# Kernel optimization log

Measured on AMD Instinct MI355X. Metric: run time of the kernel, lower is better.

The kernel has to match this reference:

```python
import jax, jax.numpy as jnp
import numpy as np

N_NODES = 100000
N_EDGES = 1600000
D = 128  # feat_input_size_node == embed_inside_size == feat_target_size


def gcn_layer(x, W, b, row, col, ew, n_nodes):
    """PyG GCNConv with scalar edge_weight, add_self_loops=True, normalize=True.
    x: [N, Fin], W: [Fout, Fin], b: [Fout], row/col: [E], ew: [E].
    Messages flow row -> col (source_to_target)."""
    h = x @ W.T  # [N, Fout]
    # degree includes self-loop weight 1.0 per node
    deg = jax.ops.segment_sum(ew, col, num_segments=n_nodes) + 1.0  # [N]
    dinv = jnp.where(deg > 0, jax.lax.rsqrt(deg), 0.0)  # [N]
    norm = dinv[row] * ew * dinv[col]  # [E]
    msgs = norm[:, None] * h[row]  # [E, Fout] -- gather
    agg = jax.ops.segment_sum(msgs, col, num_segments=n_nodes)  # scatter-add
    agg = agg + (dinv * dinv)[:, None] * h  # self-loop contribution (weight 1)
    return agg + b


def setup_inputs() -> dict:
    key = jax.random.key(0)
    k1, k2, k3, k4, k5, k6, k7 = jax.random.split(key, 7)
    edge_tuples = jax.random.randint(k1, (2, N_EDGES), 0, N_NODES, dtype=jnp.int64) if jax.config.jax_enable_x64 else jax.random.randint(k1, (2, N_EDGES), 0, N_NODES).astype(jnp.int32)
    edge_feats = jax.random.uniform(k2, (N_EDGES, 1), dtype=jnp.float32)
    node_feats = jax.random.normal(k3, (N_NODES, D), dtype=jnp.float32)
    s1 = 1.0 / np.sqrt(D)
    W1 = jax.random.uniform(k4, (D, D), minval=-s1, maxval=s1, dtype=jnp.float32)
    b1 = jnp.zeros((D,), dtype=jnp.float32)
    W2 = jax.random.uniform(k5, (D, D), minval=-s1, maxval=s1, dtype=jnp.float32)
    b2 = jnp.zeros((D,), dtype=jnp.float32)
    return {"edge_tuples": edge_tuples, "edge_feats": edge_feats, "node_feats": node_feats,
            "W1": W1, "b1": b1, "W2": W2, "b2": b2}


def reference(edge_tuples, edge_feats, node_feats, W1, b1, W2, b2):
    row, col = edge_tuples[0], edge_tuples[1]
    ew = edge_feats.squeeze(-1)  # [E]
    n = node_feats.shape[0]
    h = gcn_layer(node_feats, W1, b1, row, col, ew, n)
    h = jnp.tanh(h)  # activate='tanh' between the two GCN layers
    out = gcn_layer(h, W2, b2, row, col, ew, n)
    # skip=Identity (Fin==Fout), doskip=1
    return out + node_feats
```

## Files before the change

kernel.cpp:

```cpp
#include <hip/hip_runtime.h>
#include <hip/hip_bf16.h>
#include <math.h>

#define D 128
#define SCAN_T 256
#define EPB 4096
#define MAXNB 800

typedef unsigned long long ull;
typedef unsigned short ushort_t;
typedef __attribute__((ext_vector_type(8))) short bf16x8;
typedef __attribute__((ext_vector_type(4))) float f32x4;

__device__ __forceinline__ float bf_lo(unsigned u) { return __uint_as_float(u << 16); }
__device__ __forceinline__ float bf_hi(unsigned u) { return __uint_as_float(u & 0xffff0000u); }
__device__ __forceinline__ unsigned bpack(float a, float b) {
  unsigned ua = __float_as_uint(a), ub = __float_as_uint(b);
  ua += 0x7fff + ((ua >> 16) & 1);
  ub += 0x7fff + ((ub >> 16) & 1);
  return (ua >> 16) | (ub & 0xffff0000u);
}
__device__ __forceinline__ ushort_t bh16(float a) {
  unsigned ua = __float_as_uint(a);
  ua += 0x7fff + ((ua >> 16) & 1);
  return (ushort_t)(ua >> 16);
}

__global__ __launch_bounds__(256) void k_h1(const int* __restrict__ col, int E, int B1, int B1pad,
                                            int* __restrict__ gh, int NB,
                                            const float2* __restrict__ x2, unsigned* __restrict__ xb, int n64,
                                            const float* __restrict__ W1, const float* __restrict__ W2,
                                            ushort_t* __restrict__ Whi1, ushort_t* __restrict__ Wlo1,
                                            ushort_t* __restrict__ Whi2, ushort_t* __restrict__ Wlo2) {
  int b = blockIdx.x, t = threadIdx.x;
  if (b < B1) {
    __shared__ int h[MAXNB];
    for (int i = t; i < NB; i += 256) h[i] = 0;
    __syncthreads();
    int e0 = b * EPB, e1 = min(E, e0 + EPB);
    for (int e = e0 + t; e < e1; e += 256) atomicAdd(&h[col[e] >> 7], 1);
    __syncthreads();
    for (int i = t; i < NB; i += 256) gh[i * B1pad + b] = h[i];
    return;
  }
  int idx = (b - B1) * 256 + t;
  if (idx < n64) { float2 v = x2[idx]; xb[idx] = bpack(v.x, v.y); return; }
  int j = idx - n64;
  if (j >= 2 * D * D) return;
  const float* W = (j < D * D) ? W1 : W2;
  ushort_t* Hh = (j < D * D) ? Whi1 : Whi2;
  ushort_t* Hl = (j < D * D) ? Wlo1 : Wlo2;
  int k = j & (D * D - 1);
  float w = W[k];
  ushort_t hh = bh16(w);
  Hh[k] = hh;
  Hl[k] = bh16(w - __uint_as_float((unsigned)hh << 16));
}

__global__ __launch_bounds__(512) void k_hscan(int* __restrict__ gh, int* __restrict__ binTotal,
                                               int B1, int B1pad) {
  __shared__ int wsum[8];
  int bin = blockIdx.x, t = threadIdx.x;
  int v = (t < B1) ? gh[bin * B1pad + t] : 0;
  int lane = t & 63, wid = t >> 6;
  int x = v;
  #pragma unroll
  for (int d = 1; d < 64; d <<= 1) { int y = __shfl_up(x, d, 64); if (lane >= d) x += y; }
  if (lane == 63) wsum[wid] = x;
  __syncthreads();
  int woff = 0;
  for (int w = 0; w < wid; ++w) woff += wsum[w];
  if (t < B1) gh[bin * B1pad + t] = woff + x - v;
  if (t == 511) binTotal[bin] = woff + x;
}

__device__ __forceinline__ int block_excl_scan(int v, int t, int* wsum, int* total) {
  int lane = t & 63, wid = t >> 6;
  int x = v;
  #pragma unroll
  for (int d = 1; d < 64; d <<= 1) {
    int y = __shfl_up(x, d, 64);
    if (lane >= d) x += y;
  }
  if (lane == 63) wsum[wid] = x;
  __syncthreads();
  int woff = 0;
  for (int w = 0; w < wid; ++w) woff += wsum[w];
  if (total) { int tot = 0; for (int w = 0; w < 4; ++w) tot += wsum[w]; *total = tot; }
  return woff + x - v;
}

__global__ __launch_bounds__(SCAN_T) void k_hscan2(const int* __restrict__ binTotal,
                                                   int* __restrict__ binBase, int NB) {
  __shared__ int wsum[4];
  int t = threadIdx.x;
  int base = t * 4;
  int v[4]; int s = 0;
  #pragma unroll
  for (int u = 0; u < 4; ++u) { v[u] = (base + u < NB) ? binTotal[base + u] : 0; s += v[u]; }
  int tot;
  int excl = block_excl_scan(s, t, wsum, &tot);
  int run = excl;
  #pragma unroll
  for (int u = 0; u < 4; ++u) { if (base + u < NB) binBase[base + u] = run; run += v[u]; }
  if (t == 0) binBase[NB] = tot;
}

__global__ __launch_bounds__(256) void k_scatter(const int* __restrict__ row, const int* __restrict__ col,
                                                 const float* __restrict__ ew,
                                                 const int* __restrict__ gh, const int* __restrict__ binBase,
                                                 int B1pad, int NB,
                                                 ull* __restrict__ a_e, int E) {
  __shared__ ull recs[EPB];
  __shared__ int hist[MAXNB];
  __shared__ int cur[MAXNB];
  __shared__ int wb[MAXNB];
  __shared__ int wsum[4];
  int b = blockIdx.x, t = threadIdx.x;
  for (int i = t; i < NB; i += 256) { hist[i] = 0; cur[i] = 0; }
  __syncthreads();
  int e0 = b * EPB;
  int cnt = min(E - e0, EPB);
  ull v[16];
  #pragma unroll
  for (int k = 0; k < 16; ++k) {
    int idx = t + k * 256;
    v[k] = 0;
    if (idx < cnt) {
      int e = e0 + idx;
      int c = col[e];
      unsigned q = __float2uint_rn(ew[e] * 32767.0f);
      if (q > 32767u) q = 32767u;
      unsigned hi = ((unsigned)c << 15) | q;
      v[k] = ((ull)hi << 32) | (unsigned)row[e];
      atomicAdd(&hist[hi >> 22], 1);
    }
  }
  __syncthreads();
  int base = t * 4;
  int hv[4];
  #pragma unroll
  for (int u = 0; u < 4; ++u) hv[u] = (base + u < NB) ? hist[base + u] : 0;
  int s = hv[0] + hv[1] + hv[2] + hv[3];
  int excl = block_excl_scan(s, t, wsum, nullptr);
  int run = excl;
  #pragma unroll
  for (int u = 0; u < 4; ++u) {
    if (base + u < NB) {
      hist[base + u] = run;
      wb[base + u] = binBase[base + u] + gh[(base + u) * B1pad + b] - run;
    }
    run += hv[u];
  }
  __syncthreads();
  #pragma unroll
  for (int k = 0; k < 16; ++k) {
    if (t + k * 256 < cnt) {
      unsigned bkt = (unsigned)(v[k] >> 54);
      int idx = hist[bkt] + atomicAdd(&cur[bkt], 1);
      recs[idx] = v[k];
    }
  }
  __syncthreads();
  for (int i = t; i < cnt; i += 256) {
    ull r = recs[i];
    a_e[wb[(unsigned)(r >> 54)] + i] = r;
  }
}

__global__ __launch_bounds__(256) void k_bucket(const ull* __restrict__ a_e,
                                                const int* __restrict__ binBase,
                                                int* __restrict__ offs, float* __restrict__ deg,
                                                unsigned* __restrict__ sorted2, int N) {
  __shared__ int hist[128];
  __shared__ float wdeg[128];
  __shared__ int pfx[128];
  __shared__ int cur[128];
  int bin = blockIdx.x, t = threadIdx.x;
  if (t < 128) { hist[t] = 0; wdeg[t] = 0.f; cur[t] = 0; }
  __syncthreads();
  int s0 = binBase[bin], s1 = binBase[bin + 1];
  for (int i = s0 + t; i < s1; i += 256) {
    unsigned hi = (unsigned)(a_e[i] >> 32);
    int lc = (hi >> 15) & 127;
    atomicAdd(&hist[lc], 1);
    atomicAdd(&wdeg[lc], (float)(hi & 32767u) * (1.0f / 32767.0f));
  }
  __syncthreads();
  if (t == 0) { int run = 0; for (int i = 0; i < 128; ++i) { pfx[i] = run; run += hist[i]; } }
  __syncthreads();
  int c0 = bin << 7;
  if (t < 128 && c0 + t < N) { offs[c0 + t] = s0 + pfx[t]; deg[c0 + t] = wdeg[t]; }
  for (int i = s0 + t; i < s1; i += 256) {
    ull v = a_e[i];
    unsigned hi = (unsigned)(v >> 32);
    int lc = (hi >> 15) & 127;
    int pos = s0 + pfx[lc] + atomicAdd(&cur[lc], 1);
    sorted2[pos] = ((unsigned)v << 15) | (hi & 32767u);
  }
}

__global__ void k_dinv(const float* __restrict__ deg, float* __restrict__ dinv,
                       int* __restrict__ offs, int N, int E) {
  int i = blockIdx.x * blockDim.x + threadIdx.x;
  if (i == 0) offs[N] = E;
  if (i < N) dinv[i] = rsqrtf(deg[i] + 1.0f);
}

__global__ void k_norm(unsigned* __restrict__ el, const int* __restrict__ offs,
                       const float* __restrict__ dinv, int N) {
  int c = blockIdx.x * blockDim.x + threadIdx.x;
  if (c >= N) return;
  int s0 = offs[c], s1 = offs[c + 1];
  float dc = dinv[c] * (1.0f / 32767.0f);
  for (int i = s0; i < s1; ++i) {
    unsigned v = el[i];
    unsigned r = v >> 15;
    float nrm = dinv[r] * (float)(v & 32767u) * dc;
    unsigned q = __float2uint_rn(nrm * 32767.0f);
    if (q > 32767u) q = 32767u;
    el[i] = (r << 15) | q;
  }
}

__global__ __launch_bounds__(256) void k_agg(const unsigned* __restrict__ H2,
                                             const unsigned* __restrict__ elist,
                                             const int* __restrict__ offs, const float* __restrict__ dinv,
                                             unsigned* __restrict__ outb, int N) {
  int lane = threadIdx.x & 63;
  int c = blockIdx.x * 4 + (threadIdx.x >> 6);
  if (c >= N) return;
  int start = offs[c];
  int m = offs[c + 1] - start;
  int q = lane >> 4;
  int fi = lane & 15;
  float a0 = 0.f, a1 = 0.f, a2 = 0.f, a3 = 0.f, a4 = 0.f, a5 = 0.f, a6 = 0.f, a7 = 0.f;
  for (int base = 0; base < m; base += 64) {
    int chunk = min(64, m - base);
    unsigned rec = (lane < chunk) ? elist[start + base + lane] : 0u;
    int iters = (chunk + 3) >> 2;
    int i = 0;
    for (; i + 4 <= iters; i += 4) {
      unsigned e0 = __shfl(rec, 4 * i + q, 64);
      unsigned e1 = __shfl(rec, 4 * i + 4 + q, 64);
      unsigned e2 = __shfl(rec, 4 * i + 8 + q, 64);
      unsigned e3 = __shfl(rec, 4 * i + 12 + q, 64);
      uint4 u0 = *(const uint4*)&H2[(size_t)(e0 >> 15) * 64 + fi * 4];
      uint4 u1 = *(const uint4*)&H2[(size_t)(e1 >> 15) * 64 + fi * 4];
      uint4 u2 = *(const uint4*)&H2[(size_t)(e2 >> 15) * 64 + fi * 4];
      uint4 u3 = *(const uint4*)&H2[(size_t)(e3 >> 15) * 64 + fi * 4];
      float w0 = (float)(e0 & 0x7fffu) * (1.0f / 32767.0f);
      float w1 = (float)(e1 & 0x7fffu) * (1.0f / 32767.0f);
      float w2 = (float)(e2 & 0x7fffu) * (1.0f / 32767.0f);
      float w3 = (float)(e3 & 0x7fffu) * (1.0f / 32767.0f);
      a0 += w0 * bf_lo(u0.x); a1 += w0 * bf_hi(u0.x);
      a2 += w0 * bf_lo(u0.y); a3 += w0 * bf_hi(u0.y);
      a4 += w0 * bf_lo(u0.z); a5 += w0 * bf_hi(u0.z);
      a6 += w0 * bf_lo(u0.w); a7 += w0 * bf_hi(u0.w);
      a0 += w1 * bf_lo(u1.x); a1 += w1 * bf_hi(u1.x);
      a2 += w1 * bf_lo(u1.y); a3 += w1 * bf_hi(u1.y);
      a4 += w1 * bf_lo(u1.z); a5 += w1 * bf_hi(u1.z);
      a6 += w1 * bf_lo(u1.w); a7 += w1 * bf_hi(u1.w);
      a0 += w2 * bf_lo(u2.x); a1 += w2 * bf_hi(u2.x);
      a2 += w2 * bf_lo(u2.y); a3 += w2 * bf_hi(u2.y);
      a4 += w2 * bf_lo(u2.z); a5 += w2 * bf_hi(u2.z);
      a6 += w2 * bf_lo(u2.w); a7 += w2 * bf_hi(u2.w);
      a0 += w3 * bf_lo(u3.x); a1 += w3 * bf_hi(u3.x);
      a2 += w3 * bf_lo(u3.y); a3 += w3 * bf_hi(u3.y);
      a4 += w3 * bf_lo(u3.z); a5 += w3 * bf_hi(u3.z);
      a6 += w3 * bf_lo(u3.w); a7 += w3 * bf_hi(u3.w);
    }
    for (; i < iters; ++i) {
      unsigned e0 = __shfl(rec, 4 * i + q, 64);
      float w0 = (float)(e0 & 0x7fffu) * (1.0f / 32767.0f);
      uint4 u0 = *(const uint4*)&H2[(size_t)(e0 >> 15) * 64 + fi * 4];
      a0 += w0 * bf_lo(u0.x); a1 += w0 * bf_hi(u0.x);
      a2 += w0 * bf_lo(u0.y); a3 += w0 * bf_hi(u0.y);
      a4 += w0 * bf_lo(u0.z); a5 += w0 * bf_hi(u0.z);
      a6 += w0 * bf_lo(u0.w); a7 += w0 * bf_hi(u0.w);
    }
  }
  a0 += __shfl_xor(a0, 16, 64); a0 += __shfl_xor(a0, 32, 64);
  a1 += __shfl_xor(a1, 16, 64); a1 += __shfl_xor(a1, 32, 64);
  a2 += __shfl_xor(a2, 16, 64); a2 += __shfl_xor(a2, 32, 64);
  a3 += __shfl_xor(a3, 16, 64); a3 += __shfl_xor(a3, 32, 64);
  a4 += __shfl_xor(a4, 16, 64); a4 += __shfl_xor(a4, 32, 64);
  a5 += __shfl_xor(a5, 16, 64); a5 += __shfl_xor(a5, 32, 64);
  a6 += __shfl_xor(a6, 16, 64); a6 += __shfl_xor(a6, 32, 64);
  a7 += __shfl_xor(a7, 16, 64); a7 += __shfl_xor(a7, 32, 64);
  if (q == 0) {
    float dv = dinv[c], sw = dv * dv;
    uint4 us = *(const uint4*)&H2[(size_t)c * 64 + fi * 4];
    a0 += sw * bf_lo(us.x); a1 += sw * bf_hi(us.x);
    a2 += sw * bf_lo(us.y); a3 += sw * bf_hi(us.y);
    a4 += sw * bf_lo(us.z); a5 += sw * bf_hi(us.z);
    a6 += sw * bf_lo(us.w); a7 += sw * bf_hi(us.w);
    uint4 o;
    o.x = bpack(a0, a1); o.y = bpack(a2, a3); o.z = bpack(a4, a5); o.w = bpack(a6, a7);
    *(uint4*)&outb[(size_t)c * 64 + fi * 4] = o;
  }
}

template<int TANH, int SKIP>
__global__ __launch_bounds__(256) void k_mgemm(const ushort_t* __restrict__ S,
                                               const ushort_t* __restrict__ Whi,
                                               const ushort_t* __restrict__ Wlo,
                                               const float* __restrict__ bias,
                                               const ushort_t* __restrict__ skipb,
                                               void* __restrict__ outv, int n) {
  int wave = threadIdx.x >> 6, lane = threadIdx.x & 63;
  int cl = lane & 15;
  int kg = lane >> 4;
  int cb0 = wave * 2;

  bf16x8 bh[2][4], bl[2][4];
  float bv[2];
  #pragma unroll
  for (int c = 0; c < 2; ++c) {
    int col = (cb0 + c) * 16 + cl;
    const ushort_t* wh = Whi + (size_t)col * D + kg * 8;
    const ushort_t* wl = Wlo + (size_t)col * D + kg * 8;
    #pragma unroll
    for (int kt = 0; kt < 4; ++kt) {
      bh[c][kt] = *(const bf16x8*)(wh + kt * 32);
      bl[c][kt] = *(const bf16x8*)(wl + kt * 32);
    }
    bv[c] = bias[col];
  }

  int ntiles = (n + 15) >> 4;
  for (int t = blockIdx.x; t < ntiles; t += gridDim.x) {
    int arow = t * 16 + cl; if (arow >= n) arow = n - 1;
    const ushort_t* srow = S + (size_t)arow * D + kg * 8;
    bf16x8 a[4];
    #pragma unroll
    for (int kt = 0; kt < 4; ++kt) a[kt] = *(const bf16x8*)(srow + kt * 32);
    #pragma unroll
    for (int c = 0; c < 2; ++c) {
      f32x4 acc = {0.f, 0.f, 0.f, 0.f};
      #pragma unroll
      for (int kt = 0; kt < 4; ++kt)
        acc = __builtin_amdgcn_mfma_f32_16x16x32_bf16(a[kt], bh[c][kt], acc, 0, 0, 0);
      #pragma unroll
      for (int kt = 0; kt < 4; ++kt)
        acc = __builtin_amdgcn_mfma_f32_16x16x32_bf16(a[kt], bl[c][kt], acc, 0, 0, 0);
      int col = (cb0 + c) * 16 + cl;
      #pragma unroll
      for (int i = 0; i < 4; ++i) {
        int r = t * 16 + kg * 4 + i;
        if (r < n) {
          float o = acc[i] + bv[c];
          if (TANH) {
            o = tanhf(o);
            ((ushort_t*)outv)[(size_t)r * D + col] = bh16(o);
          } else {
            if (SKIP) o += __uint_as_float((unsigned)skipb[(size_t)r * D + col] << 16);
            ((float*)outv)[(size_t)r * D + col] = o;
          }
        }
      }
    }
  }
}

extern "C" void kernel_launch(void* const* d_in, const int* in_sizes, int n_in,
                              void* d_out, int out_size, void* d_ws, size_t ws_size,
                              hipStream_t stream) {
  const int*   et = (const int*)d_in[0];
  const float* ef = (const float*)d_in[1];
  const float* x  = (const float*)d_in[2];
  const float* W1 = (const float*)d_in[3];
  const float* b1 = (const float*)d_in[4];
  const float* W2 = (const float*)d_in[5];
  const float* b2 = (const float*)d_in[6];

  int E = in_sizes[1];
  int N = in_sizes[2] / D;
  const int* row = et;
  const int* col = et + E;

  int NB = (N + 127) >> 7;
  int B1 = (E + EPB - 1) / EPB;
  int B1pad = (B1 + 7) & ~7;

  char* p = (char*)d_ws;
  auto alloc = [&](size_t bytes) { char* q = p; p += (bytes + 255) & ~(size_t)255; return q; };
  int*      gh       = (int*)     alloc((size_t)NB * B1pad * 4);
  int*      binTotal = (int*)     alloc((size_t)NB * 4);
  int*      binBase  = (int*)     alloc((size_t)(NB + 1) * 4);
  ull*      a_e      = (ull*)     alloc((size_t)E * 8);
  unsigned* elist    = (unsigned*)alloc((size_t)E * 4);
  int*      offs     = (int*)     alloc((size_t)(N + 1) * 4);
  float*    deg      = (float*)   alloc((size_t)N * 4);
  float*    dinv     = (float*)   alloc((size_t)N * 4);
  unsigned* xb       = (unsigned*)alloc((size_t)N * 64 * 4);
  unsigned* s2b      = (unsigned*)alloc((size_t)N * 64 * 4);
  ushort_t* whi1 = (ushort_t*)alloc(D * D * 2);
  ushort_t* wlo1 = (ushort_t*)alloc(D * D * 2);
  ushort_t* whi2 = (ushort_t*)alloc(D * D * 2);
  ushort_t* wlo2 = (ushort_t*)alloc(D * D * 2);
  unsigned* doutb = (unsigned*)d_out;

  int prepBlocks = (N * 64 + 2 * D * D + 255) / 256;
  k_h1<<<B1 + prepBlocks, 256, 0, stream>>>(col, E, B1, B1pad, gh, NB,
                                            (const float2*)x, xb, N * 64,
                                            W1, W2, whi1, wlo1, whi2, wlo2);
  k_hscan<<<NB, 512, 0, stream>>>(gh, binTotal, B1, B1pad);
  k_hscan2<<<1, SCAN_T, 0, stream>>>(binTotal, binBase, NB);
  k_scatter<<<B1, 256, 0, stream>>>(row, col, ef, gh, binBase, B1pad, NB, a_e, E);
  k_bucket<<<NB, 256, 0, stream>>>(a_e, binBase, offs, deg, elist, N);
  k_dinv<<<(N + 255) / 256, 256, 0, stream>>>(deg, dinv, offs, N, E);
  k_norm<<<(N + 255) / 256, 256, 0, stream>>>(elist, offs, dinv, N);

  int ab = (N + 3) / 4;
  int gb = 1024;
  k_agg<<<ab, 256, 0, stream>>>(xb, elist, offs, dinv, doutb, N);
  k_mgemm<1, 0><<<gb, 256, 0, stream>>>((const ushort_t*)doutb, whi1, wlo1, b1, nullptr, doutb, N);
  k_agg<<<ab, 256, 0, stream>>>(doutb, elist, offs, dinv, s2b, N);
  k_mgemm<0, 1><<<gb, 256, 0, stream>>>((const ushort_t*)s2b, whi2, wlo2, b2,
                                        (const ushort_t*)xb, d_out, N);
}
```

Baseline: 259.5 us.

## Switch features and weights to fp16 with packed-half aggregation and one node per 16 lanes

Replaces bf16 storage with fp16 for node features and weights. This drops the hi/lo split-weight MFMA pass, so the GEMM now issues a single f16 MFMA chain per tile instead of two. The aggregation kernel is restructured so each node uses 16 lanes instead of a full wave, with no cross-lane reduction, and it accumulates in packed half2 FMAs flushed to fp32 every four edges. Edge rows and fp16 norms move into separate arrays, replacing the 15-bit quantized packed form. Risks are fp16 range and precision loss, both in the packed half accumulation and in feeding a single-precision-pass GEMM.

```diff
diff --git a/kernel.cpp b/kernel.cpp
--- a/kernel.cpp
+++ b/kernel.cpp
@@ -1,5 +1,4 @@
 #include <hip/hip_runtime.h>
-#include <hip/hip_bf16.h>
 #include <math.h>
 
 #define D 128
@@ -9,29 +8,23 @@
 
 typedef unsigned long long ull;
 typedef unsigned short ushort_t;
-typedef __attribute__((ext_vector_type(8))) short bf16x8;
+typedef _Float16 f16;
+typedef __attribute__((ext_vector_type(2))) _Float16 f16x2;
+typedef __attribute__((ext_vector_type(8))) _Float16 f16x8;
 typedef __attribute__((ext_vector_type(4))) float f32x4;
 
-__device__ __forceinline__ float bf_lo(unsigned u) { return __uint_as_float(u << 16); }
-__device__ __forceinline__ float bf_hi(unsigned u) { return __uint_as_float(u & 0xffff0000u); }
-__device__ __forceinline__ unsigned bpack(float a, float b) {
-  unsigned ua = __float_as_uint(a), ub = __float_as_uint(b);
-  ua += 0x7fff + ((ua >> 16) & 1);
-  ub += 0x7fff + ((ub >> 16) & 1);
-  return (ua >> 16) | (ub & 0xffff0000u);
-}
-__device__ __forceinline__ ushort_t bh16(float a) {
-  unsigned ua = __float_as_uint(a);
-  ua += 0x7fff + ((ua >> 16) & 1);
-  return (ushort_t)(ua >> 16);
-}
+__device__ __forceinline__ ushort_t f16b(float x) { f16 h = (f16)x; return __builtin_bit_cast(ushort_t, h); }
+__device__ __forceinline__ unsigned packh2(float a, float b) {
+  f16x2 v = {(f16)a, (f16)b};
+  return __builtin_bit_cast(unsigned, v);
+}
+__device__ __forceinline__ f16x2 bch2(unsigned u) { return __builtin_bit_cast(f16x2, u); }
 
 __global__ __launch_bounds__(256) void k_h1(const int* __restrict__ col, int E, int B1, int B1pad,
                                             int* __restrict__ gh, int NB,
                                             const float2* __restrict__ x2, unsigned* __restrict__ xb, int n64,
                                             const float* __restrict__ W1, const float* __restrict__ W2,
-                                            ushort_t* __restrict__ Whi1, ushort_t* __restrict__ Wlo1,
-                                            ushort_t* __restrict__ Whi2, ushort_t* __restrict__ Wlo2) {
+                                            ushort_t* __restrict__ Wf1, ushort_t* __restrict__ Wf2) {
   int b = blockIdx.x, t = threadIdx.x;
   if (b < B1) {
     __shared__ int h[MAXNB];
@@ -44,17 +37,13 @@
     return;
   }
   int idx = (b - B1) * 256 + t;
-  if (idx < n64) { float2 v = x2[idx]; xb[idx] = bpack(v.x, v.y); return; }
+  if (idx < n64) { float2 v = x2[idx]; xb[idx] = packh2(v.x, v.y); return; }
   int j = idx - n64;
   if (j >= 2 * D * D) return;
   const float* W = (j < D * D) ? W1 : W2;
-  ushort_t* Hh = (j < D * D) ? Whi1 : Whi2;
-  ushort_t* Hl = (j < D * D) ? Wlo1 : Wlo2;
+  ushort_t* Wd = (j < D * D) ? Wf1 : Wf2;
   int k = j & (D * D - 1);
-  float w = W[k];
-  ushort_t hh = bh16(w);
-  Hh[k] = hh;
-  Hl[k] = bh16(w - __uint_as_float((unsigned)hh << 16));
+  Wd[k] = f16b(W[k]);
 }
 
 __global__ __launch_bounds__(512) void k_hscan(int* __restrict__ gh, int* __restrict__ binTotal,
@@ -207,8 +196,9 @@
   if (i < N) dinv[i] = rsqrtf(deg[i] + 1.0f);
 }
 
-__global__ void k_norm(unsigned* __restrict__ el, const int* __restrict__ offs,
-                       const float* __restrict__ dinv, int N) {
+__global__ void k_norm(const unsigned* __restrict__ el, const int* __restrict__ offs,
+                       const float* __restrict__ dinv,
+                       unsigned* __restrict__ rows, unsigned* __restrict__ normp, int N) {
   int c = blockIdx.x * blockDim.x + threadIdx.x;
   if (c >= N) return;
   int s0 = offs[c], s1 = offs[c + 1];
@@ -217,94 +207,78 @@
     unsigned v = el[i];
     unsigned r = v >> 15;
     float nrm = dinv[r] * (float)(v & 32767u) * dc;
-    unsigned q = __float2uint_rn(nrm * 32767.0f);
-    if (q > 32767u) q = 32767u;
-    el[i] = (r << 15) | q;
-  }
-}
-
-__global__ __launch_bounds__(256) void k_agg(const unsigned* __restrict__ H2,
-                                             const unsigned* __restrict__ elist,
+    rows[i] = r;
+    normp[i] = (unsigned)f16b(nrm) * 0x10001u;
+  }
+}
+
+__global__ __launch_bounds__(256) void k_agg(const uint4* __restrict__ H4,
+                                             const unsigned* __restrict__ rows,
+                                             const unsigned* __restrict__ normp,
                                              const int* __restrict__ offs, const float* __restrict__ dinv,
-                                             unsigned* __restrict__ outb, int N) {
-  int lane = threadIdx.x & 63;
-  int c = blockIdx.x * 4 + (threadIdx.x >> 6);
+                                             uint4* __restrict__ out4, int N) {
+  int t = threadIdx.x;
+  int fl = t & 15;
+  int g = t >> 4;
+  int sb = ((t & 63) >> 4) * 16;
+  int c = blockIdx.x * 16 + g;
   if (c >= N) return;
   int start = offs[c];
   int m = offs[c + 1] - start;
-  int q = lane >> 4;
-  int fi = lane & 15;
-  float a0 = 0.f, a1 = 0.f, a2 = 0.f, a3 = 0.f, a4 = 0.f, a5 = 0.f, a6 = 0.f, a7 = 0.f;
-  for (int base = 0; base < m; base += 64) {
-    int chunk = min(64, m - base);
-    unsigned rec = (lane < chunk) ? elist[start + base + lane] : 0u;
-    int iters = (chunk + 3) >> 2;
-    int i = 0;
-    for (; i + 4 <= iters; i += 4) {
-      unsigned e0 = __shfl(rec, 4 * i + q, 64);
-      unsigned e1 = __shfl(rec, 4 * i + 4 + q, 64);
-      unsigned e2 = __shfl(rec, 4 * i + 8 + q, 64);
-      unsigned e3 = __shfl(rec, 4 * i + 12 + q, 64);
-      uint4 u0 = *(const uint4*)&H2[(size_t)(e0 >> 15) * 64 + fi * 4];
-      uint4 u1 = *(const uint4*)&H2[(size_t)(e1 >> 15) * 64 + fi * 4];
-      uint4 u2 = *(const uint4*)&H2[(size_t)(e2 >> 15) * 64 + fi * 4];
-      uint4 u3 = *(const uint4*)&H2[(size_t)(e3 >> 15) * 64 + fi * 4];
-      float w0 = (float)(e0 & 0x7fffu) * (1.0f / 32767.0f);
-      float w1 = (float)(e1 & 0x7fffu) * (1.0f / 32767.0f);
-      float w2 = (float)(e2 & 0x7fffu) * (1.0f / 32767.0f);
-      float w3 = (float)(e3 & 0x7fffu) * (1.0f / 32767.0f);
-      a0 += w0 * bf_lo(u0.x); a1 += w0 * bf_hi(u0.x);
-      a2 += w0 * bf_lo(u0.y); a3 += w0 * bf_hi(u0.y);
-      a4 += w0 * bf_lo(u0.z); a5 += w0 * bf_hi(u0.z);
-      a6 += w0 * bf_lo(u0.w); a7 += w0 * bf_hi(u0.w);
-      a0 += w1 * bf_lo(u1.x); a1 += w1 * bf_hi(u1.x);
-      a2 += w1 * bf_lo(u1.y); a3 += w1 * bf_hi(u1.y);
-      a4 += w1 * bf_lo(u1.z); a5 += w1 * bf_hi(u1.z);
-      a6 += w1 * bf_lo(u1.w); a7 += w1 * bf_hi(u1.w);
-      a0 += w2 * bf_lo(u2.x); a1 += w2 * bf_hi(u2.x);
-      a2 += w2 * bf_lo(u2.y); a3 += w2 * bf_hi(u2.y);
-      a4 += w2 * bf_lo(u2.z); a5 += w2 * bf_hi(u2.z);
-      a6 += w2 * bf_lo(u2.w); a7 += w2 * bf_hi(u2.w);
-      a0 += w3 * bf_lo(u3.x); a1 += w3 * bf_hi(u3.x);
-      a2 += w3 * bf_lo(u3.y); a3 += w3 * bf_hi(u3.y);
-      a4 += w3 * bf_lo(u3.z); a5 += w3 * bf_hi(u3.z);
-      a6 += w3 * bf_lo(u3.w); a7 += w3 * bf_hi(u3.w);
-    }
-    for (; i < iters; ++i) {
-      unsigned e0 = __shfl(rec, 4 * i + q, 64);
-      float w0 = (float)(e0 & 0x7fffu) * (1.0f / 32767.0f);
-      uint4 u0 = *(const uint4*)&H2[(size_t)(e0 >> 15) * 64 + fi * 4];
-      a0 += w0 * bf_lo(u0.x); a1 += w0 * bf_hi(u0.x);
-      a2 += w0 * bf_lo(u0.y); a3 += w0 * bf_hi(u0.y);
-      a4 += w0 * bf_lo(u0.z); a5 += w0 * bf_hi(u0.z);
-      a6 += w0 * bf_lo(u0.w); a7 += w0 * bf_hi(u0.w);
-    }
-  }
-  a0 += __shfl_xor(a0, 16, 64); a0 += __shfl_xor(a0, 32, 64);
-  a1 += __shfl_xor(a1, 16, 64); a1 += __shfl_xor(a1, 32, 64);
-  a2 += __shfl_xor(a2, 16, 64); a2 += __shfl_xor(a2, 32, 64);
-  a3 += __shfl_xor(a3, 16, 64); a3 += __shfl_xor(a3, 32, 64);
-  a4 += __shfl_xor(a4, 16, 64); a4 += __shfl_xor(a4, 32, 64);
-  a5 += __shfl_xor(a5, 16, 64); a5 += __shfl_xor(a5, 32, 64);
-  a6 += __shfl_xor(a6, 16, 64); a6 += __shfl_xor(a6, 32, 64);
-  a7 += __shfl_xor(a7, 16, 64); a7 += __shfl_xor(a7, 32, 64);
-  if (q == 0) {
-    float dv = dinv[c], sw = dv * dv;
-    uint4 us = *(const uint4*)&H2[(size_t)c * 64 + fi * 4];
-    a0 += sw * bf_lo(us.x); a1 += sw * bf_hi(us.x);
-    a2 += sw * bf_lo(us.y); a3 += sw * bf_hi(us.y);
-    a4 += sw * bf_lo(us.z); a5 += sw * bf_hi(us.z);
-    a6 += sw * bf_lo(us.w); a7 += sw * bf_hi(us.w);
-    uint4 o;
-    o.x = bpack(a0, a1); o.y = bpack(a2, a3); o.z = bpack(a4, a5); o.w = bpack(a6, a7);
-    *(uint4*)&outb[(size_t)c * 64 + fi * 4] = o;
-  }
+  float a0=0.f,a1=0.f,a2=0.f,a3=0.f,a4=0.f,a5=0.f,a6=0.f,a7=0.f;
+  f16x2 p0={0,0}, p1={0,0}, p2={0,0}, p3={0,0};
+  for (int eb = 0; eb < m; eb += 16) {
+    int chunk = min(16, m - eb);
+    unsigned rr = 0, wwp = 0;
+    if (fl < chunk) { rr = rows[start + eb + fl]; wwp = normp[start + eb + fl]; }
+    int j = 0;
+    for (; j + 4 <= chunk; j += 4) {
+      unsigned r0 = __shfl(rr, sb + j, 64);     unsigned w0 = __shfl(wwp, sb + j, 64);
+      unsigned r1 = __shfl(rr, sb + j + 1, 64); unsigned w1 = __shfl(wwp, sb + j + 1, 64);
+      unsigned r2 = __shfl(rr, sb + j + 2, 64); unsigned w2 = __shfl(wwp, sb + j + 2, 64);
+      unsigned r3 = __shfl(rr, sb + j + 3, 64); unsigned w3 = __shfl(wwp, sb + j + 3, 64);
+      uint4 u0 = H4[(size_t)r0 * 16 + fl];
+      uint4 u1 = H4[(size_t)r1 * 16 + fl];
+      uint4 u2 = H4[(size_t)r2 * 16 + fl];
+      uint4 u3 = H4[(size_t)r3 * 16 + fl];
+      f16x2 wv0 = bch2(w0), wv1 = bch2(w1), wv2 = bch2(w2), wv3 = bch2(w3);
+      p0 += bch2(u0.x) * wv0; p1 += bch2(u0.y) * wv0; p2 += bch2(u0.z) * wv0; p3 += bch2(u0.w) * wv0;
+      p0 += bch2(u1.x) * wv1; p1 += bch2(u1.y) * wv1; p2 += bch2(u1.z) * wv1; p3 += bch2(u1.w) * wv1;
+      p0 += bch2(u2.x) * wv2; p1 += bch2(u2.y) * wv2; p2 += bch2(u2.z) * wv2; p3 += bch2(u2.w) * wv2;
+      p0 += bch2(u3.x) * wv3; p1 += bch2(u3.y) * wv3; p2 += bch2(u3.z) * wv3; p3 += bch2(u3.w) * wv3;
+      a0 += (float)p0[0]; a1 += (float)p0[1];
+      a2 += (float)p1[0]; a3 += (float)p1[1];
+      a4 += (float)p2[0]; a5 += (float)p2[1];
+      a6 += (float)p3[0]; a7 += (float)p3[1];
+      p0 = (f16x2){0,0}; p1 = (f16x2){0,0}; p2 = (f16x2){0,0}; p3 = (f16x2){0,0};
+    }
+    for (; j < chunk; ++j) {
+      unsigned r0 = __shfl(rr, sb + j, 64); unsigned w0 = __shfl(wwp, sb + j, 64);
+      uint4 u0 = H4[(size_t)r0 * 16 + fl];
+      f16x2 wv0 = bch2(w0);
+      p0 += bch2(u0.x) * wv0; p1 += bch2(u0.y) * wv0; p2 += bch2(u0.z) * wv0; p3 += bch2(u0.w) * wv0;
+    }
+    a0 += (float)p0[0]; a1 += (float)p0[1];
+    a2 += (float)p1[0]; a3 += (float)p1[1];
+    a4 += (float)p2[0]; a5 += (float)p2[1];
+    a6 += (float)p3[0]; a7 += (float)p3[1];
+    p0 = (f16x2){0,0}; p1 = (f16x2){0,0}; p2 = (f16x2){0,0}; p3 = (f16x2){0,0};
+  }
+  float dv = dinv[c], sw = dv * dv;
+  uint4 us = H4[(size_t)c * 16 + fl];
+  f16x2 h0 = bch2(us.x), h1 = bch2(us.y), h2 = bch2(us.z), h3 = bch2(us.w);
+  a0 += sw * (float)h0[0]; a1 += sw * (float)h0[1];
+  a2 += sw * (float)h1[0]; a3 += sw * (float)h1[1];
+  a4 += sw * (float)h2[0]; a5 += sw * (float)h2[1];
+  a6 += sw * (float)h3[0]; a7 += sw * (float)h3[1];
+  uint4 o;
+  o.x = packh2(a0, a1); o.y = packh2(a2, a3); o.z = packh2(a4, a5); o.w = packh2(a6, a7);
+  out4[(size_t)c * 16 + fl] = o;
 }
 
 template<int TANH, int SKIP>
 __global__ __launch_bounds__(256) void k_mgemm(const ushort_t* __restrict__ S,
-                                               const ushort_t* __restrict__ Whi,
-                                               const ushort_t* __restrict__ Wlo,
+                                               const ushort_t* __restrict__ Wf,
                                                const float* __restrict__ bias,
                                                const ushort_t* __restrict__ skipb,
                                                void* __restrict__ outv, int n) {
@@ -313,18 +287,14 @@
   int kg = lane >> 4;
   int cb0 = wave * 2;
 
-  bf16x8 bh[2][4], bl[2][4];
+  f16x8 bfr[2][4];
   float bv[2];
   #pragma unroll
   for (int c = 0; c < 2; ++c) {
     int col = (cb0 + c) * 16 + cl;
-    const ushort_t* wh = Whi + (size_t)col * D + kg * 8;
-    const ushort_t* wl = Wlo + (size_t)col * D + kg * 8;
+    const ushort_t* wp = Wf + (size_t)col * D + kg * 8;
     #pragma unroll
-    for (int kt = 0; kt < 4; ++kt) {
-      bh[c][kt] = *(const bf16x8*)(wh + kt * 32);
-      bl[c][kt] = *(const bf16x8*)(wl + kt * 32);
-    }
+    for (int kt = 0; kt < 4; ++kt) bfr[c][kt] = *(const f16x8*)(wp + kt * 32);
     bv[c] = bias[col];
   }
 
@@ -332,18 +302,15 @@
   for (int t = blockIdx.x; t < ntiles; t += gridDim.x) {
     int arow = t * 16 + cl; if (arow >= n) arow = n - 1;
     const ushort_t* srow = S + (size_t)arow * D + kg * 8;
-    bf16x8 a[4];
+    f16x8 a[4];
     #pragma unroll
-    for (int kt = 0; kt < 4; ++kt) a[kt] = *(const bf16x8*)(srow + kt * 32);
+    for (int kt = 0; kt < 4; ++kt) a[kt] = *(const f16x8*)(srow + kt * 32);
     #pragma unroll
     for (int c = 0; c < 2; ++c) {
       f32x4 acc = {0.f, 0.f, 0.f, 0.f};
       #pragma unroll
       for (int kt = 0; kt < 4; ++kt)
-        acc = __builtin_amdgcn_mfma_f32_16x16x32_bf16(a[kt], bh[c][kt], acc, 0, 0, 0);
-      #pragma unroll
-      for (int kt = 0; kt < 4; ++kt)
-        acc = __builtin_amdgcn_mfma_f32_16x16x32_bf16(a[kt], bl[c][kt], acc, 0, 0, 0);
+        acc = __builtin_amdgcn_mfma_f32_16x16x32_f16(a[kt], bfr[c][kt], acc, 0, 0, 0);
       int col = (cb0 + c) * 16 + cl;
       #pragma unroll
       for (int i = 0; i < 4; ++i) {
@@ -352,9 +319,9 @@
           float o = acc[i] + bv[c];
           if (TANH) {
             o = tanhf(o);
-            ((ushort_t*)outv)[(size_t)r * D + col] = bh16(o);
+            ((ushort_t*)outv)[(size_t)r * D + col] = f16b(o);
           } else {
-            if (SKIP) o += __uint_as_float((unsigned)skipb[(size_t)r * D + col] << 16);
+            if (SKIP) o += (float)((const f16*)skipb)[(size_t)r * D + col];
             ((float*)outv)[(size_t)r * D + col] = o;
           }
         }
@@ -395,28 +362,28 @@
   float*    dinv     = (float*)   alloc((size_t)N * 4);
   unsigned* xb       = (unsigned*)alloc((size_t)N * 64 * 4);
   unsigned* s2b      = (unsigned*)alloc((size_t)N * 64 * 4);
-  ushort_t* whi1 = (ushort_t*)alloc(D * D * 2);
-  ushort_t* wlo1 = (ushort_t*)alloc(D * D * 2);
-  ushort_t* whi2 = (ushort_t*)alloc(D * D * 2);
-  ushort_t* wlo2 = (ushort_t*)alloc(D * D * 2);
+  ushort_t* wf1 = (ushort_t*)alloc(D * D * 2);
+  ushort_t* wf2 = (ushort_t*)alloc(D * D * 2);
+  unsigned* rows  = (unsigned*)a_e;
+  unsigned* normp = rows + E;
   unsigned* doutb = (unsigned*)d_out;
 
   int prepBlocks = (N * 64 + 2 * D * D + 255) / 256;
   k_h1<<<B1 + prepBlocks, 256, 0, stream>>>(col, E, B1, B1pad, gh, NB,
                                             (const float2*)x, xb, N * 64,
-                                            W1, W2, whi1, wlo1, whi2, wlo2);
+                                            W1, W2, wf1, wf2);
   k_hscan<<<NB, 512, 0, stream>>>(gh, binTotal, B1, B1pad);
   k_hscan2<<<1, SCAN_T, 0, stream>>>(binTotal, binBase, NB);
   k_scatter<<<B1, 256, 0, stream>>>(row, col, ef, gh, binBase, B1pad, NB, a_e, E);
   k_bucket<<<NB, 256, 0, stream>>>(a_e, binBase, offs, deg, elist, N);
   k_dinv<<<(N + 255) / 256, 256, 0, stream>>>(deg, dinv, offs, N, E);
-  k_norm<<<(N + 255) / 256, 256, 0, stream>>>(elist, offs, dinv, N);
-
-  int ab = (N + 3) / 4;
+  k_norm<<<(N + 255) / 256, 256, 0, stream>>>(elist, offs, dinv, rows, normp, N);
+
+  int ab = (N + 15) / 16;
   int gb = 1024;
-  k_agg<<<ab, 256, 0, stream>>>(xb, elist, offs, dinv, doutb, N);
-  k_mgemm<1, 0><<<gb, 256, 0, stream>>>((const ushort_t*)doutb, whi1, wlo1, b1, nullptr, doutb, N);
-  k_agg<<<ab, 256, 0, stream>>>(doutb, elist, offs, dinv, s2b, N);
-  k_mgemm<0, 1><<<gb, 256, 0, stream>>>((const ushort_t*)s2b, whi2, wlo2, b2,
+  k_agg<<<ab, 256, 0, stream>>>((const uint4*)xb, rows, normp, offs, dinv, (uint4*)doutb, N);
+  k_mgemm<1, 0><<<gb, 256, 0, stream>>>((const ushort_t*)doutb, wf1, b1, nullptr, doutb, N);
+  k_agg<<<ab, 256, 0, stream>>>((const uint4*)doutb, rows, normp, offs, dinv, (uint4*)s2b, N);
+  k_mgemm<0, 1><<<gb, 256, 0, stream>>>((const ushort_t*)s2b, wf2, b2,
                                         (const ushort_t*)xb, d_out, N);
 }
```

Measured after the change: 258.0 us. Within noise of the previous version (-0.6%).
